# Kernel optimization log

Hardware: AMD Instinct MI355X
Metric: run time of the kernel (lower is better)

The kernel has to match this reference:

```python
import jax, jax.numpy as jnp
import numpy as np

D_MODEL = 1024
N_HEADS = 16
D_HEAD = D_MODEL // N_HEADS


def setup_inputs() -> dict:
    key = jax.random.key(0)
    ks = jax.random.split(key, 5)
    scale = 1.0 / np.sqrt(D_MODEL)
    return {
        "x": jax.random.normal(ks[0], (2, 2048, D_MODEL), dtype=jnp.float32),
        "W_q": jax.random.normal(ks[1], (D_MODEL, D_MODEL), dtype=jnp.float32) * scale,
        "W_k": jax.random.normal(ks[2], (D_MODEL, D_MODEL), dtype=jnp.float32) * scale,
        "W_v": jax.random.normal(ks[3], (D_MODEL, D_MODEL), dtype=jnp.float32) * scale,
        "W_o": jax.random.normal(ks[4], (D_MODEL, D_MODEL), dtype=jnp.float32) * scale,
    }


def reference(x, W_q, W_k, W_v, W_o):
    B, S, _ = x.shape
    # nn.Linear computes x @ W.T; weights stored [out, in]
    def proj(W):
        y = jnp.einsum("bsd,ed->bse", x, W)
        return y.reshape(B, S, N_HEADS, D_HEAD).transpose(0, 2, 1, 3)  # [B,H,S,Dh]

    q, k, v = proj(W_q), proj(W_k), proj(W_v)
    scores = jnp.einsum("bhqd,bhkd->bhqk", q, k) / jnp.sqrt(jnp.float32(D_HEAD))
    causal = jnp.triu(jnp.ones((S, S), dtype=bool), k=1)
    scores = jnp.where(causal, -jnp.inf, scores)
    attn = jax.nn.softmax(scores, axis=-1)
    out = jnp.einsum("bhqk,bhkd->bhqd", attn, v)  # [B,H,S,Dh]
    out = out.transpose(0, 2, 1, 3).reshape(B, S, D_MODEL)
    return jnp.einsum("bsd,ed->bse", out, W_o)
```

## Files before the change

kernel.cpp:

```cpp
#include <hip/hip_runtime.h>


#define DMODEL 1024
#define NHEADS 16
#define DHEAD  64
#define SEQ    2048
#define BATCH  2
#define MROWS  (BATCH * SEQ)

typedef __bf16 bf16x8 __attribute__((ext_vector_type(8)));
typedef __bf16 bf16x4 __attribute__((ext_vector_type(4)));
typedef float  f32x4  __attribute__((ext_vector_type(4)));

__device__ __forceinline__ f32x4 mfma16(bf16x8 a, bf16x8 b, f32x4 c) {
    return __builtin_amdgcn_mfma_f32_16x16x32_bf16(a, b, c, 0, 0, 0);
}

__device__ __forceinline__ bf16x8 ld8(const float* p) {
    const f32x4 a0 = *(const f32x4*)p;
    const f32x4 a1 = *(const f32x4*)(p + 4);
    bf16x8 v;
    v[0] = (__bf16)a0[0]; v[1] = (__bf16)a0[1];
    v[2] = (__bf16)a0[2]; v[3] = (__bf16)a0[3];
    v[4] = (__bf16)a1[0]; v[5] = (__bf16)a1[1];
    v[6] = (__bf16)a1[2]; v[7] = (__bf16)a1[3];
    return v;
}

__device__ __forceinline__ void gll16(const __bf16* g, __bf16* l) {
    __builtin_amdgcn_global_load_lds(
        (const __attribute__((address_space(1))) void*)g,
        (__attribute__((address_space(3))) void*)l,
        16, 0, 0);
}

__global__ __launch_bounds__(256) void cvt_kernel(const float* __restrict__ x,
                                                  const float* __restrict__ Wq,
                                                  const float* __restrict__ Wk,
                                                  const float* __restrict__ Wv,
                                                  const float* __restrict__ Wo,
                                                  __bf16* __restrict__ xb,
                                                  __bf16* __restrict__ wcat) {
    const int y = blockIdx.y;
    const float* src;
    __bf16* dst;
    int nchunks;
    if (y == 0) { src = x; dst = xb; nchunks = (MROWS * DMODEL) / 8; }
    else {
        src = (y == 1) ? Wq : (y == 2) ? Wk : (y == 3) ? Wv : Wo;
        dst = wcat + (size_t)(y - 1) * DMODEL * DMODEL;
        nchunks = (DMODEL * DMODEL) / 8;
    }
    const int c = blockIdx.x * 256 + threadIdx.x;
    if (c < nchunks) *(bf16x8*)(dst + (size_t)c * 8) = ld8(src + (size_t)c * 8);
}

template <typename TC>
__device__ __forceinline__ void gemm_bb_body(const __bf16* __restrict__ A,
                                             const __bf16* __restrict__ W,
                                             TC* __restrict__ C,
                                             __bf16* __restrict__ VT,
                                             bool vt, int m0, int n0,
                                             float scale) {
    constexpr int K = DMODEL;
    __shared__ __align__(16) __bf16 As[128][32];
    __shared__ __align__(16) __bf16 Bs[128][32];

    const int tid  = threadIdx.x;
    const int lane = tid & 63;
    const int wave = tid >> 6;
    const int quad = lane >> 4;
    const int l16  = lane & 15;
    const int wm   = wave & 1;
    const int wn   = wave >> 1;

    const int srow = lane >> 2;
    const int scol = (lane & 3) * 8;

    const __bf16* a0p = A + (size_t)(m0 + wave * 16 + srow) * K + scol;
    const __bf16* a1p = A + (size_t)(m0 + 64 + wave * 16 + srow) * K + scol;
    const __bf16* b0p = W + (size_t)(n0 + wave * 16 + srow) * K + scol;
    const __bf16* b1p = W + (size_t)(n0 + 64 + wave * 16 + srow) * K + scol;

    f32x4 acc[4][4] = {};

    for (int k0 = 0; k0 < K; k0 += 32) {
        __syncthreads();
        gll16(a0p + k0, &As[wave * 16][0]);
        gll16(a1p + k0, &As[64 + wave * 16][0]);
        gll16(b0p + k0, &Bs[wave * 16][0]);
        gll16(b1p + k0, &Bs[64 + wave * 16][0]);
        __syncthreads();

        bf16x8 af[4], bfr[4];
#pragma unroll
        for (int i = 0; i < 4; ++i) {
            af[i]  = *(const bf16x8*)(&As[wm * 64 + i * 16 + l16][quad * 8]);
            bfr[i] = *(const bf16x8*)(&Bs[wn * 64 + i * 16 + l16][quad * 8]);
        }
#pragma unroll
        for (int mi = 0; mi < 4; ++mi)
#pragma unroll
            for (int ni = 0; ni < 4; ++ni)
                acc[mi][ni] = mfma16(af[mi], bfr[ni], acc[mi][ni]);
    }

    if (!vt) {
#pragma unroll
        for (int mi = 0; mi < 4; ++mi)
#pragma unroll
            for (int ni = 0; ni < 4; ++ni)
#pragma unroll
                for (int r = 0; r < 4; ++r) {
                    int row = m0 + wm * 64 + mi * 16 + quad * 4 + r;
                    int col = n0 + wn * 64 + ni * 16 + l16;
                    C[(size_t)row * DMODEL + col] = (TC)(acc[mi][ni][r] * scale);
                }
    } else {
#pragma unroll
        for (int mi = 0; mi < 4; ++mi)
#pragma unroll
            for (int ni = 0; ni < 4; ++ni) {
                const int m  = m0 + wm * 64 + mi * 16 + quad * 4;
                const int hd = n0 + wn * 64 + ni * 16 + l16;
                bf16x4 v4;
#pragma unroll
                for (int r = 0; r < 4; ++r) v4[r] = (__bf16)acc[mi][ni][r];
                *(bf16x4*)(VT + (size_t)hd * MROWS + m) = v4;
            }
    }
}

#define QSCALE 0.1803368801111204f

__global__ __launch_bounds__(256) void qkv_kernel(const __bf16* __restrict__ X,
                                                  const __bf16* __restrict__ wcat,
                                                  __bf16* __restrict__ Q,
                                                  __bf16* __restrict__ K,
                                                  __bf16* __restrict__ VT) {
    const int z = blockIdx.z;
    const __bf16* W = wcat + (size_t)z * DMODEL * DMODEL;
    __bf16* Y = (z == 0) ? Q : K;
    const float scale = (z == 0) ? QSCALE : 1.0f;
    gemm_bb_body<__bf16>(X, W, Y, VT, z == 2,
                         blockIdx.y * 128, blockIdx.x * 128, scale);
}

__global__ __launch_bounds__(256) void out_gemm_kernel(const __bf16* __restrict__ A,
                                                       const __bf16* __restrict__ W,
                                                       float* __restrict__ C) {
    gemm_bb_body<float>(A, W, C, nullptr, false,
                        blockIdx.y * 128, blockIdx.x * 128, 1.0f);
}

__global__ __launch_bounds__(128) void attn_kernel(const __bf16* __restrict__ Q,
                                                   const __bf16* __restrict__ Kg,
                                                   const __bf16* __restrict__ VTg,
                                                   __bf16* __restrict__ O) {
    const int bh = blockIdx.x;
    const int qt = 63 - blockIdx.y;
    const int b = bh >> 4, h = bh & 15;
    const size_t base = (size_t)b * SEQ * DMODEL + (size_t)h * DHEAD;

    const int tid  = threadIdx.x;
    const int lane = tid & 63;
    const int wave = tid >> 6;
    const int quad = lane >> 4;
    const int l16  = lane & 15;

    __shared__ __align__(16) __bf16 Ks[64][64];
    __shared__ __align__(16) __bf16 Vs[64][64];
    __shared__ __align__(16) __bf16 Ps[2][2][16][40];

    const int sr = lane >> 3;
    const int sc = ((lane & 7) ^ sr) * 8;

    const int qrow = qt * 32 + wave * 16 + l16;

    const bf16x8 qf0 = *(const bf16x8*)(Q + base + (size_t)qrow * DMODEL + quad * 8);
    const bf16x8 qf1 = *(const bf16x8*)(Q + base + (size_t)qrow * DMODEL + 32 + quad * 8);

    const __bf16* kgp = Kg + base;
    const __bf16* vgp = VTg + (size_t)(h * 64) * MROWS + (size_t)b * SEQ;

    f32x4 oacc[4] = {};
    float m_i = -1e30f, l_i = 0.f;

    const int ntiles = qt / 2 + 1;
    const int gsw = (l16 & 7);

    for (int kt = 0; kt < ntiles; ++kt) {
        const int k0 = kt * 64;
        __syncthreads();
#pragma unroll
        for (int j = 0; j < 4; ++j) {
            const int row = wave * 32 + j * 8;
            gll16(kgp + (size_t)(k0 + row + sr) * DMODEL + sc, &Ks[row][0]);
            gll16(vgp + (size_t)(row + sr) * MROWS + k0 + sc, &Vs[row][0]);
        }
        __syncthreads();

        const bool diag = (kt == ntiles - 1);

        f32x4 s[4];
#pragma unroll
        for (int g = 0; g < 4; ++g) {
            const bf16x8 kfa = *(const bf16x8*)(&Ks[g * 16 + l16][(quad ^ gsw) * 8]);
            const bf16x8 kfb = *(const bf16x8*)(&Ks[g * 16 + l16][((quad + 4) ^ gsw) * 8]);
            f32x4 t = {};
            t = mfma16(kfa, qf0, t);
            t = mfma16(kfb, qf1, t);
            s[g] = t;
        }

        float mx;
        bool ok[4][4];
        if (!diag) {
            mx = s[0][0];
#pragma unroll
            for (int g = 0; g < 4; ++g)
#pragma unroll
                for (int r = 0; r < 4; ++r) mx = fmaxf(mx, s[g][r]);
        } else {
            mx = -1e30f;
#pragma unroll
            for (int g = 0; g < 4; ++g)
#pragma unroll
                for (int r = 0; r < 4; ++r) {
                    const int kk = k0 + g * 16 + quad * 4 + r;
                    ok[g][r] = (kk <= qrow);
                    mx = fmaxf(mx, ok[g][r] ? s[g][r] : -1e30f);
                }
        }
        mx = fmaxf(mx, __shfl_xor(mx, 16));
        mx = fmaxf(mx, __shfl_xor(mx, 32));

        const bool defer = __all(mx - m_i <= 8.0f);
        float mnew;
        if (defer) {
            mnew = m_i;
        } else {
            mnew = fmaxf(m_i, mx);
            const float alpha = exp2f(m_i - mnew);
            m_i = mnew;
#pragma unroll
            for (int f = 0; f < 4; ++f) oacc[f] *= alpha;
            l_i *= alpha;
        }

        float rs = 0.f;
        bf16x4 w4[4];
        if (!diag) {
#pragma unroll
            for (int g = 0; g < 4; ++g)
#pragma unroll
                for (int r = 0; r < 4; ++r) {
                    const float p = exp2f(s[g][r] - mnew);
                    rs += p;
                    w4[g][r] = (__bf16)p;
                }
        } else {
#pragma unroll
            for (int g = 0; g < 4; ++g)
#pragma unroll
                for (int r = 0; r < 4; ++r) {
                    const float p = ok[g][r] ? exp2f(s[g][r] - mnew) : 0.f;
                    rs += p;
                    w4[g][r] = (__bf16)p;
                }
        }
        rs += __shfl_xor(rs, 16);
        rs += __shfl_xor(rs, 32);
        l_i += rs;

#pragma unroll
        for (int g = 0; g < 4; ++g)
            *(bf16x4*)(&Ps[wave][g >> 1][l16][(g & 1) * 16 + quad * 4]) = w4[g];

        const bf16x8 pf0 = *(const bf16x8*)(&Ps[wave][0][l16][quad * 8]);
        const bf16x8 pf1 = *(const bf16x8*)(&Ps[wave][1][l16][quad * 8]);
#pragma unroll
        for (int f = 0; f < 4; ++f) {
            const bf16x8 vfa = *(const bf16x8*)(&Vs[f * 16 + l16][(quad ^ gsw) * 8]);
            const bf16x8 vfb = *(const bf16x8*)(&Vs[f * 16 + l16][((quad + 4) ^ gsw) * 8]);
            f32x4 t = oacc[f];
            t = mfma16(vfa, pf0, t);
            t = mfma16(vfb, pf1, t);
            oacc[f] = t;
        }
    }

    const float inv = (l_i > 0.f) ? (1.f / l_i) : 0.f;
#pragma unroll
    for (int f = 0; f < 4; ++f) {
        bf16x4 o;
#pragma unroll
        for (int r = 0; r < 4; ++r) o[r] = (__bf16)(oacc[f][r] * inv);
        *(bf16x4*)(O + base + (size_t)qrow * DMODEL + f * 16 + quad * 4) = o;
    }
}

extern "C" void kernel_launch(void* const* d_in, const int* in_sizes, int n_in,
                              void* d_out, int out_size, void* d_ws, size_t ws_size,
                              hipStream_t stream) {
    const float* x  = (const float*)d_in[0];
    const float* Wq = (const float*)d_in[1];
    const float* Wk = (const float*)d_in[2];
    const float* Wv = (const float*)d_in[3];
    const float* Wo = (const float*)d_in[4];
    float* out = (float*)d_out;

    const size_t tm = (size_t)MROWS * DMODEL;
    const size_t tw = (size_t)DMODEL * DMODEL;
    __bf16* Q    = (__bf16*)d_ws;
    __bf16* K    = Q + tm;
    __bf16* VT   = K + tm;
    __bf16* xb   = VT + tm;
    __bf16* wcat = xb + tm;

    dim3 gc(2048, 5);
    cvt_kernel<<<gc, 256, 0, stream>>>(x, Wq, Wk, Wv, Wo, xb, wcat);

    dim3 g1(DMODEL / 128, MROWS / 128, 3);
    qkv_kernel<<<g1, 256, 0, stream>>>(xb, wcat, Q, K, VT);

    dim3 g2(BATCH * NHEADS, SEQ / 32);
    attn_kernel<<<g2, 128, 0, stream>>>(Q, K, VT, Q);

    dim3 g3(DMODEL / 128, MROWS / 128);
    out_gemm_kernel<<<g3, 256, 0, stream>>>(Q, wcat + 3 * tw, out);
}
```

Measured before the change: 191.7 us.

## Split long causal attention rows across two blocks and merge with combine kernel

The attention kernel now uses 64-row query tiles with 4 waves. The 16 longest query tiles per head have their key range split in half across two blocks. Each half writes a normalized partial output plus its max and sum into reused workspace, and a new combine kernel merges the two halves. This is meant to even out causal load imbalance and shorten the tail. The QKV GEMM grid is also flattened from a z-dimension into a wider x-dimension. The cost is an extra kernel launch and extra global traffic for the partials.

```diff
diff --git a/kernel.cpp b/kernel.cpp
--- a/kernel.cpp
+++ b/kernel.cpp
@@ -60,7 +60,7 @@
                                              const __bf16* __restrict__ W,
                                              TC* __restrict__ C,
                                              __bf16* __restrict__ VT,
-                                             bool vt, int m0, int n0,
+                                             bool vt, int m0, int bn0, int cn0,
                                              float scale) {
     constexpr int K = DMODEL;
     __shared__ __align__(16) __bf16 As[128][32];
@@ -79,8 +79,8 @@
 
     const __bf16* a0p = A + (size_t)(m0 + wave * 16 + srow) * K + scol;
     const __bf16* a1p = A + (size_t)(m0 + 64 + wave * 16 + srow) * K + scol;
-    const __bf16* b0p = W + (size_t)(n0 + wave * 16 + srow) * K + scol;
-    const __bf16* b1p = W + (size_t)(n0 + 64 + wave * 16 + srow) * K + scol;
+    const __bf16* b0p = W + (size_t)(bn0 + wave * 16 + srow) * K + scol;
+    const __bf16* b1p = W + (size_t)(bn0 + 64 + wave * 16 + srow) * K + scol;
 
     f32x4 acc[4][4] = {};
 
@@ -113,7 +113,7 @@
 #pragma unroll
                 for (int r = 0; r < 4; ++r) {
                     int row = m0 + wm * 64 + mi * 16 + quad * 4 + r;
-                    int col = n0 + wn * 64 + ni * 16 + l16;
+                    int col = cn0 + wn * 64 + ni * 16 + l16;
                     C[(size_t)row * DMODEL + col] = (TC)(acc[mi][ni][r] * scale);
                 }
     } else {
@@ -122,7 +122,7 @@
 #pragma unroll
             for (int ni = 0; ni < 4; ++ni) {
                 const int m  = m0 + wm * 64 + mi * 16 + quad * 4;
-                const int hd = n0 + wn * 64 + ni * 16 + l16;
+                const int hd = cn0 + wn * 64 + ni * 16 + l16;
                 bf16x4 v4;
 #pragma unroll
                 for (int r = 0; r < 4; ++r) v4[r] = (__bf16)acc[mi][ni][r];
@@ -138,27 +138,38 @@
                                                   __bf16* __restrict__ Q,
                                                   __bf16* __restrict__ K,
                                                   __bf16* __restrict__ VT) {
-    const int z = blockIdx.z;
-    const __bf16* W = wcat + (size_t)z * DMODEL * DMODEL;
+    const int bn0 = blockIdx.x * 128;
+    const int z   = bn0 >> 10;
+    const int cn0 = bn0 - (z << 10);
     __bf16* Y = (z == 0) ? Q : K;
     const float scale = (z == 0) ? QSCALE : 1.0f;
-    gemm_bb_body<__bf16>(X, W, Y, VT, z == 2,
-                         blockIdx.y * 128, blockIdx.x * 128, scale);
+    gemm_bb_body<__bf16>(X, wcat, Y, VT, z == 2,
+                         blockIdx.y * 128, bn0, cn0, scale);
 }
 
 __global__ __launch_bounds__(256) void out_gemm_kernel(const __bf16* __restrict__ A,
                                                        const __bf16* __restrict__ W,
                                                        float* __restrict__ C) {
     gemm_bb_body<float>(A, W, C, nullptr, false,
-                        blockIdx.y * 128, blockIdx.x * 128, 1.0f);
-}
-
-__global__ __launch_bounds__(128) void attn_kernel(const __bf16* __restrict__ Q,
+                        blockIdx.y * 128, blockIdx.x * 128, blockIdx.x * 128, 1.0f);
+}
+
+__global__ __launch_bounds__(256) void attn_kernel(const __bf16* __restrict__ Q,
                                                    const __bf16* __restrict__ Kg,
                                                    const __bf16* __restrict__ VTg,
-                                                   __bf16* __restrict__ O) {
+                                                   __bf16* __restrict__ O,
+                                                   __bf16* __restrict__ On,
+                                                   float2* __restrict__ ml) {
     const int bh = blockIdx.x;
-    const int qt = 63 - blockIdx.y;
+    const int y  = blockIdx.y;
+    int qt2, zz = 0;
+    bool split;
+    if (y < 32) { split = true;  qt2 = 31 - (y >> 1); zz = y & 1; }
+    else        { split = false; qt2 = 47 - y; }
+    const int n = qt2 + 1;
+    int kt0 = 0, kt1 = n;
+    if (split) { const int hh = (n + 1) >> 1; if (zz) kt0 = hh; else kt1 = hh; }
+
     const int b = bh >> 4, h = bh & 15;
     const size_t base = (size_t)b * SEQ * DMODEL + (size_t)h * DHEAD;
 
@@ -170,12 +181,12 @@
 
     __shared__ __align__(16) __bf16 Ks[64][64];
     __shared__ __align__(16) __bf16 Vs[64][64];
-    __shared__ __align__(16) __bf16 Ps[2][2][16][40];
+    __shared__ __align__(16) __bf16 Ps[4][2][16][40];
 
     const int sr = lane >> 3;
     const int sc = ((lane & 7) ^ sr) * 8;
 
-    const int qrow = qt * 32 + wave * 16 + l16;
+    const int qrow = qt2 * 64 + wave * 16 + l16;
 
     const bf16x8 qf0 = *(const bf16x8*)(Q + base + (size_t)qrow * DMODEL + quad * 8);
     const bf16x8 qf1 = *(const bf16x8*)(Q + base + (size_t)qrow * DMODEL + 32 + quad * 8);
@@ -186,21 +197,20 @@
     f32x4 oacc[4] = {};
     float m_i = -1e30f, l_i = 0.f;
 
-    const int ntiles = qt / 2 + 1;
     const int gsw = (l16 & 7);
 
-    for (int kt = 0; kt < ntiles; ++kt) {
+    for (int kt = kt0; kt < kt1; ++kt) {
         const int k0 = kt * 64;
         __syncthreads();
 #pragma unroll
-        for (int j = 0; j < 4; ++j) {
-            const int row = wave * 32 + j * 8;
+        for (int j = 0; j < 2; ++j) {
+            const int row = wave * 16 + j * 8;
             gll16(kgp + (size_t)(k0 + row + sr) * DMODEL + sc, &Ks[row][0]);
             gll16(vgp + (size_t)(row + sr) * MROWS + k0 + sc, &Vs[row][0]);
         }
         __syncthreads();
 
-        const bool diag = (kt == ntiles - 1);
+        const bool diag = (kt == n - 1);
 
         f32x4 s[4];
 #pragma unroll
@@ -291,13 +301,56 @@
     }
 
     const float inv = (l_i > 0.f) ? (1.f / l_i) : 0.f;
-#pragma unroll
-    for (int f = 0; f < 4; ++f) {
-        bf16x4 o;
-#pragma unroll
-        for (int r = 0; r < 4; ++r) o[r] = (__bf16)(oacc[f][r] * inv);
-        *(bf16x4*)(O + base + (size_t)qrow * DMODEL + f * 16 + quad * 4) = o;
-    }
+    if (!split) {
+#pragma unroll
+        for (int f = 0; f < 4; ++f) {
+            bf16x4 o;
+#pragma unroll
+            for (int r = 0; r < 4; ++r) o[r] = (__bf16)(oacc[f][r] * inv);
+            *(bf16x4*)(O + base + (size_t)qrow * DMODEL + f * 16 + quad * 4) = o;
+        }
+    } else {
+        const int sp = qrow - 1024;
+        __bf16* dst = On + ((size_t)((zz * BATCH + b) * 1024 + sp)) * DMODEL + h * 64;
+#pragma unroll
+        for (int f = 0; f < 4; ++f) {
+            bf16x4 o;
+#pragma unroll
+            for (int r = 0; r < 4; ++r) o[r] = (__bf16)(oacc[f][r] * inv);
+            *(bf16x4*)(dst + f * 16 + quad * 4) = o;
+        }
+        if (quad == 0)
+            ml[((size_t)(zz * BATCH + b) * NHEADS + h) * 1024 + sp] =
+                make_float2(m_i, l_i);
+    }
+}
+
+__global__ __launch_bounds__(256) void combine_kernel(const __bf16* __restrict__ On,
+                                                      const float2* __restrict__ ml,
+                                                      __bf16* __restrict__ O) {
+    const int c = blockIdx.x * 256 + threadIdx.x;
+    const int e = c * 8;
+    const int b   = e >> 20;
+    const int rem = e & ((1 << 20) - 1);
+    const int sp  = rem >> 10;
+    const int col = rem & 1023;
+    const int h   = col >> 6;
+
+    const float2 ml0 = ml[((size_t)b * NHEADS + h) * 1024 + sp];
+    const float2 ml1 = ml[((size_t)(BATCH + b) * NHEADS + h) * 1024 + sp];
+    const float m  = fmaxf(ml0.x, ml1.x);
+    const float w0 = exp2f(ml0.x - m) * ml0.y;
+    const float w1 = exp2f(ml1.x - m) * ml1.y;
+    const float inv = 1.f / (w0 + w1);
+    const float a0 = w0 * inv, a1 = w1 * inv;
+
+    const bf16x8 o0 = *(const bf16x8*)(On + ((size_t)b * 1024 + sp) * DMODEL + col);
+    const bf16x8 o1 = *(const bf16x8*)(On + ((size_t)(BATCH * 1024) + b * 1024 + sp) * DMODEL + col);
+    bf16x8 o;
+#pragma unroll
+    for (int r = 0; r < 8; ++r)
+        o[r] = (__bf16)(a0 * (float)o0[r] + a1 * (float)o1[r]);
+    *(bf16x8*)(O + ((size_t)b * SEQ + 1024 + sp) * DMODEL + col) = o;
 }
 
 extern "C" void kernel_launch(void* const* d_in, const int* in_sizes, int n_in,
@@ -321,11 +374,14 @@
     dim3 gc(2048, 5);
     cvt_kernel<<<gc, 256, 0, stream>>>(x, Wq, Wk, Wv, Wo, xb, wcat);
 
-    dim3 g1(DMODEL / 128, MROWS / 128, 3);
+    dim3 g1(3072 / 128, MROWS / 128);
     qkv_kernel<<<g1, 256, 0, stream>>>(xb, wcat, Q, K, VT);
 
-    dim3 g2(BATCH * NHEADS, SEQ / 32);
-    attn_kernel<<<g2, 128, 0, stream>>>(Q, K, VT, Q);
+    dim3 g2(BATCH * NHEADS, 48);
+    attn_kernel<<<g2, 256, 0, stream>>>(Q, K, VT, Q,
+                                        xb, (float2*)wcat);
+
+    combine_kernel<<<1024, 256, 0, stream>>>(xb, (const float2*)wcat, Q);
 
     dim3 g3(DMODEL / 128, MROWS / 128);
     out_gemm_kernel<<<g3, 256, 0, stream>>>(Q, wcat + 3 * tw, out);
```

Result: slower. 199.7 us (+4.2%).
